# Kernel tuning notes

Hardware: AMD Instinct MI355X
Metric: run time of the kernel (lower is better)

## Reference

```python
import jax, jax.numpy as jnp
from jax import lax
import numpy as np

B, N, H, K = 64, 256, 1024, 3  # batch, num_proposals, hidden_dim, conv kernel size
LN_EPS = 1e-5


def setup_inputs() -> dict:
    key = jax.random.key(0)
    k1, k2, k3 = jax.random.split(key, 3)
    scale = 1.0 / np.sqrt(H)
    return {
        "f": jax.random.normal(k1, (B, N, H), dtype=jnp.float32),
        "k": jax.random.normal(k2, (B, N, H), dtype=jnp.float32),
        "W_lin": jax.random.normal(k3, (N * K, H), dtype=jnp.float32) * scale,
        "b_lin": jnp.zeros((N * K,), dtype=jnp.float32),
        "ln_gamma": jnp.ones((H,), dtype=jnp.float32),
        "ln_beta": jnp.zeros((H,), dtype=jnp.float32),
    }


def _conv_one(x, w):
    # x: [N, H] (channels, length); w: [N_out, N_in, K]
    # PyTorch F.conv1d is cross-correlation, same as lax conv with no flip.
    y = lax.conv_general_dilated(
        x[None], w, window_strides=(1,), padding="SAME",
        dimension_numbers=("NCH", "OIH", "NCH"))
    return y[0]  # [N, H]


def reference(f, k, W_lin, b_lin, ln_gamma, ln_beta):
    # Dynamic weight generation: [B, N, H] -> [B, N, N*K] -> [B, N, N, K]
    weight = jnp.einsum("bnh,oh->bno", f, W_lin) + b_lin
    weight = weight.reshape(B, N, N, K)
    # Per-sample dynamic conv1d over the hidden dim (batched via vmap)
    out = jax.vmap(_conv_one)(k, weight)  # [B, N, H]
    # LayerNorm over hidden dim
    mu = jnp.mean(out, axis=-1, keepdims=True)
    var = jnp.var(out, axis=-1, keepdims=True)
    out = (out - mu) * lax.rsqrt(var + LN_EPS) * ln_gamma + ln_beta
    return out
```

## Files before the change

kernel.cpp:

```cpp
#include <hip/hip_runtime.h>
#include <math.h>

#define Bsz 64
#define Nn  256
#define Hh  1024
#define NK  768

typedef __bf16 bf16;
typedef bf16 bf16x4 __attribute__((ext_vector_type(4)));
typedef bf16 bf16x8 __attribute__((ext_vector_type(8)));
typedef float floatx4 __attribute__((ext_vector_type(4)));

#define KT_ROWS   1026
#define KT_BSTRIDE (KT_ROWS * 256)

__device__ __forceinline__ void gl_lds16(const bf16* g, bf16* l) {
    __builtin_amdgcn_global_load_lds(
        (__attribute__((address_space(1))) void*)(g),
        (__attribute__((address_space(3))) void*)(l), 16, 0, 0);
}

__global__ __launch_bounds__(256) void prep_kernel(
    const float* __restrict__ f, const float* __restrict__ wl,
    const float* __restrict__ kin,
    bf16* __restrict__ fbf, bf16* __restrict__ wlbf, bf16* __restrict__ kTp)
{
    __shared__ bf16 T[128 * 72];
    const int tid = threadIdx.x;
    const int bid = blockIdx.x;

    if (bid >= 2048) {
        const int STR = 524288;
        const int u0  = (bid - 2048) * 256 + tid;
        float4 a[8];
        #pragma unroll
        for (int k = 0; k < 4; ++k) {
            const float4* s4 = (const float4*)f + ((size_t)(u0 + k * STR) * 2);
            a[2 * k]     = s4[0];
            a[2 * k + 1] = s4[1];
        }
        float4 b0, b1;
        const bool doW = (u0 < 98304);
        if (doW) {
            const float4* s4 = (const float4*)wl + ((size_t)u0 * 2);
            b0 = s4[0];
            b1 = s4[1];
        }
        #pragma unroll
        for (int k = 0; k < 4; ++k) {
            bf16x8 o = {(bf16)a[2*k].x, (bf16)a[2*k].y, (bf16)a[2*k].z, (bf16)a[2*k].w,
                        (bf16)a[2*k+1].x, (bf16)a[2*k+1].y, (bf16)a[2*k+1].z, (bf16)a[2*k+1].w};
            ((bf16x8*)fbf)[u0 + k * STR] = o;
        }
        if (doW) {
            bf16x8 o = {(bf16)b0.x, (bf16)b0.y, (bf16)b0.z, (bf16)b0.w,
                        (bf16)b1.x, (bf16)b1.y, (bf16)b1.z, (bf16)b1.w};
            ((bf16x8*)wlbf)[u0] = o;
        }
        return;
    }

    const int hb = bid & 7, ib = (bid >> 3) & 3, b = bid >> 5;
    const int i0 = ib * 64, h0 = hb * 128;
    const float* src = kin + ((size_t)b << 18);
    bf16* dstb = kTp + (size_t)b * KT_BSTRIDE;

    if (hb == 0 && ib == 0) {
        dstb[tid] = (bf16)0.f;
        dstb[(size_t)1025 * 256 + tid] = (bf16)0.f;
    }
    float4 v[8];
    #pragma unroll
    for (int j = 0; j < 8; ++j) {
        int s  = tid + j * 256;
        int il = s >> 5;
        int c8 = s & 31;
        v[j] = *(const float4*)&src[(size_t)(i0 + il) * Hh + h0 + c8 * 4];
    }
    #pragma unroll
    for (int j = 0; j < 8; ++j) {
        int s  = tid + j * 256;
        int il = s >> 5;
        int c8 = s & 31;
        T[(c8      ) * 72 + il] = (bf16)v[j].x;
        T[(32 + c8 ) * 72 + il] = (bf16)v[j].y;
        T[(64 + c8 ) * 72 + il] = (bf16)v[j].z;
        T[(96 + c8 ) * 72 + il] = (bf16)v[j].w;
    }
    __syncthreads();
    #pragma unroll
    for (int p = 0; p < 4; ++p) {
        int hl = (tid >> 3) + p * 32;
        int q  = tid & 7;
        int pr = ((hl & 3) << 5) | (hl >> 2);
        bf16x8 w = *(const bf16x8*)&T[pr * 72 + q * 8];
        *(bf16x8*)&dstb[(size_t)(h0 + hl + 1) * 256 + i0 + q * 8] = w;
    }
}

__global__ __launch_bounds__(256) void gemm1_mfma(
    const bf16* __restrict__ A,
    const bf16* __restrict__ Bw,
    const float* __restrict__ bias,
    bf16* __restrict__ wgt3)
{
    __shared__ bf16 smem[25600];
    bf16* As = smem;
    bf16* Bs = smem + 8192;
    const int tid  = threadIdx.x;
    const int wave = tid >> 6, lane = tid & 63;
    const int row0 = blockIdx.y * 128;
    const int col0 = blockIdx.x * 192;

    const bf16* gA[4]; bf16* lA[4];
    #pragma unroll
    for (int j = 0; j < 4; ++j) {
        int s = tid + j * 256;
        int reg = s >> 9, rem = s & 511, row = rem >> 2, quad = rem & 3;
        gA[j] = A + (size_t)(row0 + row) * Hh + reg * 32 + quad * 8;
        lA[j] = As + s * 8;
    }
    const bf16* gB[6]; bf16* lB[6];
    #pragma unroll
    for (int j = 0; j < 6; ++j) {
        int s = tid + j * 256;
        int reg = s / 768, rem = s - reg * 768, row = rem >> 2, quad = rem & 3;
        gB[j] = Bw + (size_t)(col0 + row) * Hh + reg * 32 + quad * 8;
        lB[j] = Bs + s * 8;
    }

    const int wm = wave & 1, wn = wave >> 1;
    const int fm = lane & 15, koct = (lane >> 4) * 8;

    floatx4 zero = {0.f, 0.f, 0.f, 0.f};
    floatx4 acc[4][6];
    #pragma unroll
    for (int i = 0; i < 4; ++i)
        #pragma unroll
        for (int j = 0; j < 6; ++j) acc[i][j] = zero;

    for (int k0 = 0; k0 < Hh; k0 += 64) {
        #pragma unroll
        for (int j = 0; j < 4; ++j) gl_lds16(gA[j] + k0, lA[j]);
        #pragma unroll
        for (int j = 0; j < 6; ++j) gl_lds16(gB[j] + k0, lB[j]);
        __syncthreads();
        #pragma unroll
        for (int q = 0; q < 2; ++q) {
            bf16x8 af[4], bfr[6];
            #pragma unroll
            for (int mt = 0; mt < 4; ++mt)
                af[mt] = *(const bf16x8*)&As[q * 4096 + (wm * 64 + mt * 16 + fm) * 32 + koct];
            #pragma unroll
            for (int nt = 0; nt < 6; ++nt)
                bfr[nt] = *(const bf16x8*)&Bs[q * 6144 + (wn * 96 + nt * 16 + fm) * 32 + koct];
            #pragma unroll
            for (int mt = 0; mt < 4; ++mt)
                #pragma unroll
                for (int nt = 0; nt < 6; ++nt)
                    acc[mt][nt] = __builtin_amdgcn_mfma_f32_16x16x32_bf16(
                        af[mt], bfr[nt], acc[mt][nt], 0, 0, 0);
        }
        __syncthreads();
    }

    const int b  = row0 >> 8;
    const int nb = row0 & 255;
    bf16* Cs = smem;
    #pragma unroll
    for (int nt = 0; nt < 6; ++nt) {
        int c = wn * 96 + nt * 16 + fm;
        float bl = bias[col0 + c];
        #pragma unroll
        for (int mt = 0; mt < 4; ++mt) {
            int rb = wm * 64 + mt * 16 + (lane >> 4) * 4;
            #pragma unroll
            for (int r = 0; r < 4; ++r)
                Cs[(rb + r) * 200 + c] = (bf16)(acc[mt][nt][r] + bl);
        }
    }
    __syncthreads();
    const int i0 = blockIdx.x * 64;
    #pragma unroll
    for (int j = 0; j < 12; ++j) {
        int s = tid + j * 256;
        int t = s >> 10, rem = s & 1023, n = rem >> 3, q8 = rem & 7;
        bf16x8 v;
        #pragma unroll
        for (int u = 0; u < 8; ++u)
            v[u] = Cs[n * 200 + (q8 * 8 + u) * 3 + t];
        *(bf16x8*)&wgt3[((size_t)(b * 3 + t) << 16) + ((size_t)(nb + n) << 8) + i0 + q8 * 8] = v;
    }
}

__global__ __launch_bounds__(256, 3) void conv_mfma(
    const bf16* __restrict__ kTp,
    const bf16* __restrict__ wgt3,
    bf16* __restrict__ cbuf)
{
    __shared__ bf16 As[6144];
    __shared__ bf16 Ks[8256];
    const int tid  = threadIdx.x;
    const int wave = tid >> 6, lane = tid & 63;
    const int b  = blockIdx.z;
    const int o0 = blockIdx.y * 64;
    const int h0 = blockIdx.x * 256;
    const int wm = wave & 1, wn = wave >> 1;
    const int fm = lane & 15, koct = (lane >> 4) * 8;

    const bf16* gA[3]; bf16* lA[3];
    #pragma unroll
    for (int j = 0; j < 3; ++j) {
        int s = tid + j * 256;
        int t = s >> 8, rem = s & 255, o = rem >> 2, iq = rem & 3;
        gA[j] = wgt3 + ((size_t)(b * 3 + t) << 16) + ((size_t)(o0 + o) << 8) + iq * 8;
        lA[j] = As + s * 8;
    }
    const bf16* kb = kTp + (size_t)b * KT_BSTRIDE;
    const bf16* gK[4]; bf16* lK[4];
    #pragma unroll
    for (int j = 0; j < 4; ++j) {
        int s = tid + j * 256;
        int r = s >> 2, quad = s & 3;
        gK[j] = kb + (size_t)(h0 + r) * 256 + quad * 8;
        lK[j] = Ks + s * 8;
    }

    floatx4 zero = {0.f, 0.f, 0.f, 0.f};
    floatx4 acc[2][8];
    #pragma unroll
    for (int i = 0; i < 2; ++i)
        #pragma unroll
        for (int j = 0; j < 8; ++j) acc[i][j] = zero;

    for (int ic = 0; ic < 8; ++ic) {
        const int i0 = ic * 32;
        __syncthreads();
        #pragma unroll
        for (int j = 0; j < 3; ++j) gl_lds16(gA[j] + i0, lA[j]);
        #pragma unroll
        for (int j = 0; j < 4; ++j) gl_lds16(gK[j] + i0, lK[j]);
        if (tid < 8) {
            int r = 256 + (tid >> 2), q = tid & 3;
            bf16x8 v = *(const bf16x8*)&kb[(size_t)(h0 + r) * 256 + i0 + q * 8];
            *(bf16x8*)&Ks[r * 32 + q * 8] = v;
        }
        __syncthreads();
        #pragma unroll
        for (int t = 0; t < 3; ++t) {
            bf16x8 af[2], bfr[8];
            #pragma unroll
            for (int mt = 0; mt < 2; ++mt)
                af[mt] = *(const bf16x8*)&As[t * 2048 + (wm * 32 + mt * 16 + fm) * 32 + koct];
            #pragma unroll
            for (int nt = 0; nt < 8; ++nt)
                bfr[nt] = *(const bf16x8*)&Ks[(wn * 128 + nt * 16 + fm + t) * 32 + koct];
            #pragma unroll
            for (int mt = 0; mt < 2; ++mt)
                #pragma unroll
                for (int nt = 0; nt < 8; ++nt)
                    acc[mt][nt] = __builtin_amdgcn_mfma_f32_16x16x32_bf16(
                        af[mt], bfr[nt], acc[mt][nt], 0, 0, 0);
        }
    }

    #pragma unroll
    for (int mt = 0; mt < 2; ++mt) {
        int o = o0 + wm * 32 + mt * 16 + (lane >> 4) * 4;
        #pragma unroll
        for (int nt = 0; nt < 8; ++nt) {
            int h = h0 + wn * 128 + nt * 16 + fm;
            #pragma unroll
            for (int r = 0; r < 4; ++r)
                cbuf[((size_t)(b * 256 + o + r) << 10) + h] = (bf16)acc[mt][nt][r];
        }
    }
}

__global__ __launch_bounds__(256) void ln_kernel(
    const bf16* __restrict__ cbuf, const float* __restrict__ gamma,
    const float* __restrict__ beta, float* __restrict__ out)
{
    const int tid  = threadIdx.x;
    const int t    = tid & 127;
    const int half = tid >> 7;
    bf16x8 v[4];
    #pragma unroll
    for (int it = 0; it < 4; ++it) {
        const int row = (blockIdx.x << 3) + it * 2 + half;
        v[it] = *(const bf16x8*)(cbuf + ((size_t)row << 10) + t * 8);
    }
    float4 g0  = ((const float4*)gamma)[t * 2];
    float4 g1  = ((const float4*)gamma)[t * 2 + 1];
    float4 be0 = ((const float4*)beta)[t * 2];
    float4 be1 = ((const float4*)beta)[t * 2 + 1];
    __shared__ float r1[2][4], r2[2][4];
    #pragma unroll
    for (int it = 0; it < 4; ++it) {
        const int row = (blockIdx.x << 3) + it * 2 + half;
        float x[8];
        float s1 = 0.f, s2 = 0.f;
        #pragma unroll
        for (int u = 0; u < 8; ++u) {
            x[u] = (float)v[it][u];
            s1 += x[u];
            s2 += x[u] * x[u];
        }
        #pragma unroll
        for (int m = 1; m < 64; m <<= 1) {
            s1 += __shfl_xor(s1, m, 64);
            s2 += __shfl_xor(s2, m, 64);
        }
        const int p = it & 1;
        if ((tid & 63) == 0) { r1[p][tid >> 6] = s1; r2[p][tid >> 6] = s2; }
        __syncthreads();
        float S1 = r1[p][2 * half] + r1[p][2 * half + 1];
        float S2 = r2[p][2 * half] + r2[p][2 * half + 1];
        float mu   = S1 * (1.0f / 1024.0f);
        float var  = S2 * (1.0f / 1024.0f) - mu * mu;
        float rstd = rsqrtf(var + 1e-5f);
        float4 o0, o1;
        o0.x = (x[0] - mu) * rstd * g0.x + be0.x;
        o0.y = (x[1] - mu) * rstd * g0.y + be0.y;
        o0.z = (x[2] - mu) * rstd * g0.z + be0.z;
        o0.w = (x[3] - mu) * rstd * g0.w + be0.w;
        o1.x = (x[4] - mu) * rstd * g1.x + be1.x;
        o1.y = (x[5] - mu) * rstd * g1.y + be1.y;
        o1.z = (x[6] - mu) * rstd * g1.z + be1.z;
        o1.w = (x[7] - mu) * rstd * g1.w + be1.w;
        float* orow = out + ((size_t)row << 10) + t * 8;
        ((float4*)orow)[0] = o0;
        ((float4*)orow)[1] = o1;
    }
}

extern "C" void kernel_launch(void* const* d_in, const int* in_sizes, int n_in,
                              void* d_out, int out_size, void* d_ws, size_t ws_size,
                              hipStream_t stream) {
    const float* f     = (const float*)d_in[0];
    const float* kin   = (const float*)d_in[1];
    const float* W_lin = (const float*)d_in[2];
    const float* b_lin = (const float*)d_in[3];
    const float* gamma = (const float*)d_in[4];
    const float* beta  = (const float*)d_in[5];
    float* out = (float*)d_out;

    char* ws = (char*)d_ws;
    bf16* fbf  = (bf16*)(ws);
    bf16* cbuf = (bf16*)(ws);
    bf16* wlbf = (bf16*)(ws + 33554432);
    bf16* kTp  = (bf16*)(ws + 35127296);
    bf16* wgt3 = (bf16*)(ws + 68747264);

    prep_kernel<<<4096, 256, 0, stream>>>(f, W_lin, kin, fbf, wlbf, kTp);
    gemm1_mfma<<<dim3(4, 128), 256, 0, stream>>>(fbf, wlbf, b_lin, wgt3);
    conv_mfma<<<dim3(4, 4, 64), 256, 0, stream>>>(kTp, wgt3, cbuf);
    ln_kernel<<<2048, 256, 0, stream>>>(cbuf, gamma, beta, out);
}
```

Before: 273.2 us.

## Split prep into transpose and cast kernels; transpose via direct global-to-LDS loads

The fused prep kernel becomes two launches: a transpose of k to bf16 and a separate cast of f and W_lin to bf16. The transpose stages fp32 tiles into LDS with global_load_lds and an XOR swizzle, then converts to bf16 on readout. This removes register staging and per-element LDS stores. The cast kernel adds a sched_barrier so all loads are issued before conversion. The cost is one extra kernel launch, a larger fp32 LDS tile that may lower occupancy, and scalar strided LDS reads during readout.

```diff
diff --git a/kernel.cpp b/kernel.cpp
--- a/kernel.cpp
+++ b/kernel.cpp
@@ -19,47 +19,18 @@
         (__attribute__((address_space(1))) void*)(g),
         (__attribute__((address_space(3))) void*)(l), 16, 0, 0);
 }
-
-__global__ __launch_bounds__(256) void prep_kernel(
-    const float* __restrict__ f, const float* __restrict__ wl,
-    const float* __restrict__ kin,
-    bf16* __restrict__ fbf, bf16* __restrict__ wlbf, bf16* __restrict__ kTp)
-{
-    __shared__ bf16 T[128 * 72];
+__device__ __forceinline__ void gl_lds16f(const float* g, float* l) {
+    __builtin_amdgcn_global_load_lds(
+        (__attribute__((address_space(1))) void*)(g),
+        (__attribute__((address_space(3))) void*)(l), 16, 0, 0);
+}
+
+__global__ __launch_bounds__(256) void transpose_kernel(
+    const float* __restrict__ kin, bf16* __restrict__ kTp)
+{
+    __shared__ float Tf[64 * 128];
     const int tid = threadIdx.x;
     const int bid = blockIdx.x;
-
-    if (bid >= 2048) {
-        const int STR = 524288;
-        const int u0  = (bid - 2048) * 256 + tid;
-        float4 a[8];
-        #pragma unroll
-        for (int k = 0; k < 4; ++k) {
-            const float4* s4 = (const float4*)f + ((size_t)(u0 + k * STR) * 2);
-            a[2 * k]     = s4[0];
-            a[2 * k + 1] = s4[1];
-        }
-        float4 b0, b1;
-        const bool doW = (u0 < 98304);
-        if (doW) {
-            const float4* s4 = (const float4*)wl + ((size_t)u0 * 2);
-            b0 = s4[0];
-            b1 = s4[1];
-        }
-        #pragma unroll
-        for (int k = 0; k < 4; ++k) {
-            bf16x8 o = {(bf16)a[2*k].x, (bf16)a[2*k].y, (bf16)a[2*k].z, (bf16)a[2*k].w,
-                        (bf16)a[2*k+1].x, (bf16)a[2*k+1].y, (bf16)a[2*k+1].z, (bf16)a[2*k+1].w};
-            ((bf16x8*)fbf)[u0 + k * STR] = o;
-        }
-        if (doW) {
-            bf16x8 o = {(bf16)b0.x, (bf16)b0.y, (bf16)b0.z, (bf16)b0.w,
-                        (bf16)b1.x, (bf16)b1.y, (bf16)b1.z, (bf16)b1.w};
-            ((bf16x8*)wlbf)[u0] = o;
-        }
-        return;
-    }
-
     const int hb = bid & 7, ib = (bid >> 3) & 3, b = bid >> 5;
     const int i0 = ib * 64, h0 = hb * 128;
     const float* src = kin + ((size_t)b << 18);
@@ -69,32 +40,60 @@
         dstb[tid] = (bf16)0.f;
         dstb[(size_t)1025 * 256 + tid] = (bf16)0.f;
     }
-    float4 v[8];
     #pragma unroll
     for (int j = 0; j < 8; ++j) {
-        int s  = tid + j * 256;
-        int il = s >> 5;
-        int c8 = s & 31;
-        v[j] = *(const float4*)&src[(size_t)(i0 + il) * Hh + h0 + c8 * 4];
-    }
-    #pragma unroll
-    for (int j = 0; j < 8; ++j) {
-        int s  = tid + j * 256;
-        int il = s >> 5;
-        int c8 = s & 31;
-        T[(c8      ) * 72 + il] = (bf16)v[j].x;
-        T[(32 + c8 ) * 72 + il] = (bf16)v[j].y;
-        T[(64 + c8 ) * 72 + il] = (bf16)v[j].z;
-        T[(96 + c8 ) * 72 + il] = (bf16)v[j].w;
+        int c  = tid + j * 256;
+        int il = c >> 5;
+        int hq = (c & 31) ^ j;
+        gl_lds16f(src + (size_t)(i0 + il) * Hh + h0 + hq * 4, Tf + c * 4);
     }
     __syncthreads();
+    const int q = tid & 7;
     #pragma unroll
     for (int p = 0; p < 4; ++p) {
         int hl = (tid >> 3) + p * 32;
-        int q  = tid & 7;
-        int pr = ((hl & 3) << 5) | (hl >> 2);
-        bf16x8 w = *(const bf16x8*)&T[pr * 72 + q * 8];
-        *(bf16x8*)&dstb[(size_t)(h0 + hl + 1) * 256 + i0 + q * 8] = w;
+        bf16x8 o;
+        #pragma unroll
+        for (int j = 0; j < 8; ++j) {
+            int i = q * 8 + j;
+            float v = Tf[i * 128 + (((hl >> 2) ^ q) << 2) + (hl & 3)];
+            o[j] = (bf16)v;
+        }
+        *(bf16x8*)&dstb[(size_t)(h0 + hl + 1) * 256 + i0 + q * 8] = o;
+    }
+}
+
+__global__ __launch_bounds__(256) void cast_kernel(
+    const float* __restrict__ f, const float* __restrict__ wl,
+    bf16* __restrict__ fbf, bf16* __restrict__ wlbf)
+{
+    const int STR = 524288;
+    const int u0  = blockIdx.x * 256 + threadIdx.x;
+    float4 a[8];
+    #pragma unroll
+    for (int k = 0; k < 4; ++k) {
+        const float4* s4 = (const float4*)f + ((size_t)(u0 + k * STR) * 2);
+        a[2 * k]     = s4[0];
+        a[2 * k + 1] = s4[1];
+    }
+    float4 b0, b1;
+    const bool doW = (u0 < 98304);
+    if (doW) {
+        const float4* s4 = (const float4*)wl + ((size_t)u0 * 2);
+        b0 = s4[0];
+        b1 = s4[1];
+    }
+    __builtin_amdgcn_sched_barrier(0);
+    #pragma unroll
+    for (int k = 0; k < 4; ++k) {
+        bf16x8 o = {(bf16)a[2*k].x, (bf16)a[2*k].y, (bf16)a[2*k].z, (bf16)a[2*k].w,
+                    (bf16)a[2*k+1].x, (bf16)a[2*k+1].y, (bf16)a[2*k+1].z, (bf16)a[2*k+1].w};
+        ((bf16x8*)fbf)[u0 + k * STR] = o;
+    }
+    if (doW) {
+        bf16x8 o = {(bf16)b0.x, (bf16)b0.y, (bf16)b0.z, (bf16)b0.w,
+                    (bf16)b1.x, (bf16)b1.y, (bf16)b1.z, (bf16)b1.w};
+        ((bf16x8*)wlbf)[u0] = o;
     }
 }
 
@@ -352,7 +351,8 @@
     bf16* kTp  = (bf16*)(ws + 35127296);
     bf16* wgt3 = (bf16*)(ws + 68747264);
 
-    prep_kernel<<<4096, 256, 0, stream>>>(f, W_lin, kin, fbf, wlbf, kTp);
+    transpose_kernel<<<2048, 256, 0, stream>>>(kin, kTp);
+    cast_kernel<<<2048, 256, 0, stream>>>(f, W_lin, fbf, wlbf);
     gemm1_mfma<<<dim3(4, 128), 256, 0, stream>>>(fbf, wlbf, b_lin, wgt3);
     conv_mfma<<<dim3(4, 4, 64), 256, 0, stream>>>(kTp, wgt3, cbuf);
     ln_kernel<<<2048, 256, 0, stream>>>(cbuf, gamma, beta, out);
```

Measured after the change: 274.9 us. Within noise of the previous version (+0.6%).
